# Optimization experiments

Hardware: AMD Instinct MI355X
Metric: run time of the kernel (lower is better)

The kernel has to match this reference:

```python
import jax, jax.numpy as jnp
import numpy as np

B, T, D, H = 4, 2048, 1024, 16
Dh = D // H  # 64


def setup_inputs() -> dict:
    key = jax.random.key(0)
    ks = jax.random.split(key, 12)
    s = 1.0 / np.sqrt(D)
    return {
        "q": jax.random.normal(ks[0], (B, T, D), jnp.float32),
        "k": jax.random.normal(ks[1], (B, T, D), jnp.float32),
        "v": jax.random.normal(ks[2], (B, T, D), jnp.float32),
        "Wq": jax.random.normal(ks[3], (D, D), jnp.float32) * s,
        "bq": jnp.zeros((D,), jnp.float32),
        "Wk": jax.random.normal(ks[4], (D, D), jnp.float32) * s,
        "bk": jnp.zeros((D,), jnp.float32),
        "Wv": jax.random.normal(ks[5], (Dh, D), jnp.float32) * s,
        "bv": jnp.zeros((Dh,), jnp.float32),
        "Wo": jax.random.normal(ks[6], (D, D), jnp.float32) * s,
        "bo": jnp.zeros((D,), jnp.float32),
    }


def reference(q, k, v, Wq, bq, Wk, bk, Wv, bv, Wo, bo):
    # Projections (torch Linear: y = x @ W.T + b)
    Q = (q @ Wq.T + bq).reshape(B, T, H, Dh)   # [B,T,H,Dh]
    K = (k @ Wk.T + bk).reshape(B, T, H, Dh)   # [B,T,H,Dh]
    Vs = v @ Wv.T + bv                         # [B,T,Dh] shared across heads
    scale = 1.0 / np.sqrt(Dh).astype(np.float32)
    scores = jnp.einsum('bqhd,bkhd->bhqk', Q, K) * scale  # [B,H,T,T]
    attn = jax.nn.softmax(scores, axis=-1)
    # shared-V: broadcast V over heads
    out = jnp.einsum('bhqk,bkd->bqhd', attn, Vs)  # [B,T,H,Dh]
    out = out.reshape(B, T, D)
    y = out @ Wo.T + bo                           # [B,T,D]
    return y, attn.mean(axis=1)                   # per-head-averaged attention
```

## Files before the change

### kernel.cpp

```cpp
#include <hip/hip_runtime.h>
#include <cstdint>
#include <cstddef>

typedef __attribute__((ext_vector_type(8))) _Float16 half8;
typedef __attribute__((ext_vector_type(4))) _Float16 half4;
typedef __attribute__((ext_vector_type(4))) float f32x4;

#define DEV static __device__ __forceinline__
#define AS1(p) (const __attribute__((address_space(1))) void*)(p)
#define AS3(p) (__attribute__((address_space(3))) void*)(p)

DEV half8 cvt8(const float* p) {
    f32x4 a = *(const f32x4*)p;
    f32x4 b = *(const f32x4*)(p + 4);
    half8 o;
    o[0] = (_Float16)a[0]; o[1] = (_Float16)a[1];
    o[2] = (_Float16)a[2]; o[3] = (_Float16)a[3];
    o[4] = (_Float16)b[0]; o[5] = (_Float16)b[1];
    o[6] = (_Float16)b[2]; o[7] = (_Float16)b[3];
    return o;
}

__global__ __launch_bounds__(256)
void cvt_kernel(const float* __restrict__ in, _Float16* __restrict__ out, int n8)
{
    int i = blockIdx.x * 256 + threadIdx.x;
    int stride = gridDim.x * 256;
    for (; i < n8; i += stride)
        ((half8*)out)[i] = cvt8(in + (size_t)i * 8);
}

__global__ __launch_bounds__(256)
void opsum_kernel(const _Float16* __restrict__ a, const _Float16* __restrict__ b,
                  _Float16* __restrict__ out, int n8)
{
    int i = blockIdx.x * 256 + threadIdx.x;
    int stride = gridDim.x * 256;
    for (; i < n8; i += stride) {
        half8 x = ((const half8*)a)[i];
        half8 y = ((const half8*)b)[i];
        half8 o;
#pragma unroll
        for (int j = 0; j < 8; j++) o[j] = (_Float16)((float)x[j] + (float)y[j]);
        ((half8*)out)[i] = o;
    }
}

__global__ __launch_bounds__(256)
void combine_kernel(const _Float16* __restrict__ a, const _Float16* __restrict__ b,
                    float* __restrict__ out, int n8)
{
    int i = blockIdx.x * 256 + threadIdx.x;
    int stride = gridDim.x * 256;
    for (; i < n8; i += stride) {
        half8 x = ((const half8*)a)[i];
        half8 y = ((const half8*)b)[i];
        f32x4 o0, o1;
#pragma unroll
        for (int j = 0; j < 4; j++) o0[j] = ((float)x[j] + (float)y[j]) * 0.0625f;
#pragma unroll
        for (int j = 0; j < 4; j++) o1[j] = ((float)x[j + 4] + (float)y[j + 4]) * 0.0625f;
        *(f32x4*)(out + (size_t)i * 8) = o0;
        *(f32x4*)(out + (size_t)i * 8 + 4) = o1;
    }
}

template<bool OUT_F16>
__global__ __launch_bounds__(256, 2)
void gemm16(const _Float16* __restrict__ A, const _Float16* __restrict__ B,
            const float* __restrict__ bias, float scale, void* __restrict__ Cout,
            int M, int N, int K)
{
    __shared__ half8 As[2][512];
    __shared__ half8 Bs[2][512];
    const int tid = threadIdx.x, l = tid & 63, w = tid >> 6;
    const int lr = l & 15, lh = l >> 4;
    const int wm0 = (w >> 1) * 64, wn0 = (w & 1) * 64;
    const int bm0 = blockIdx.x * 128, bn0 = blockIdx.y * 128;
    const int nsteps = K >> 5;

    f32x4 acc[4][4] = {};

#define STAGE(buf, t) do {                                                        \
        int k0 = (t) << 5;                                                        \
        _Pragma("unroll")                                                         \
        for (int q2 = 0; q2 < 2; q2++) {                                          \
            int r = q2 * 64 + l;                                                  \
            __builtin_amdgcn_global_load_lds(                                     \
                AS1(A + (size_t)(bm0 + r) * K + k0 + w * 8),                      \
                AS3(&As[buf][w * 128 + q2 * 64]), 16, 0, 0);                      \
            __builtin_amdgcn_global_load_lds(                                     \
                AS1(B + (size_t)(bn0 + r) * K + k0 + w * 8),                      \
                AS3(&Bs[buf][w * 128 + q2 * 64]), 16, 0, 0);                      \
        }                                                                         \
    } while (0)

    STAGE(0, 0);
    __syncthreads();
    for (int t = 0; t < nsteps; t++) {
        int cur = t & 1;
        if (t + 1 < nsteps) STAGE(cur ^ 1, t + 1);
        half8 a[4], b[4];
#pragma unroll
        for (int m = 0; m < 4; m++) a[m] = As[cur][lh * 128 + wm0 + m * 16 + lr];
#pragma unroll
        for (int n = 0; n < 4; n++) b[n] = Bs[cur][lh * 128 + wn0 + n * 16 + lr];
#pragma unroll
        for (int m = 0; m < 4; m++)
#pragma unroll
            for (int n = 0; n < 4; n++)
                acc[m][n] = __builtin_amdgcn_mfma_f32_16x16x32_f16(a[m], b[n], acc[m][n], 0, 0, 0);
        __syncthreads();
    }
#undef STAGE

#pragma unroll
    for (int m = 0; m < 4; m++)
#pragma unroll
        for (int n = 0; n < 4; n++) {
            int row0 = bm0 + wm0 + m * 16 + lh * 4;
            int col = bn0 + wn0 + n * 16 + lr;
            float bv = bias[col];
#pragma unroll
            for (int j = 0; j < 4; j++) {
                float val = (acc[m][n][j] + bv) * scale;
                int row = row0 + j;
                if constexpr (OUT_F16)
                    ((_Float16*)Cout)[(size_t)row * N + col] = (_Float16)val;
                else
                    ((float*)Cout)[(size_t)row * N + col] = val;
            }
        }
}

template<int BM, int BN, int WR, int WC>
__global__ __launch_bounds__(256, 2)
void gemm_vp(const float* __restrict__ Aptr, const float* __restrict__ Bw,
             const float* __restrict__ bias, _Float16* __restrict__ Cout, int M, int N, int K)
{
    constexpr int BK = 32;
    constexpr int WM = BM / WR, WN = BN / WC;
    constexpr int MF = WM / 16, NF = WN / 16;
    constexpr int LDT = 40;
    __shared__ _Float16 Asl[BM][LDT];
    __shared__ _Float16 Bsl[BN][LDT];

    const int tid = threadIdx.x;
    const int l = tid & 63;
    const int w = tid >> 6;
    const int wr = w / WC, wc = w % WC;
    const int lr = l & 15, lh = l >> 4;
    const int bm0 = blockIdx.y * BM, bn0 = blockIdx.x * BN;

    f32x4 acc[MF][NF] = {};

    for (int k0 = 0; k0 < K; k0 += BK) {
        __syncthreads();
        for (int c = tid; c < BM * 4; c += 256) {
            int row = c >> 2, c8 = (c & 3) << 3;
            *(half8*)&Asl[row][c8] = cvt8(Aptr + (size_t)(bm0 + row) * K + k0 + c8);
        }
        for (int c = tid; c < BN * 4; c += 256) {
            int row = c >> 2, c8 = (c & 3) << 3;
            *(half8*)&Bsl[row][c8] = cvt8(Bw + (size_t)(bn0 + row) * K + k0 + c8);
        }
        __syncthreads();

        half8 a[MF], b[NF];
#pragma unroll
        for (int m = 0; m < MF; m++)
            a[m] = *(const half8*)&Asl[wr * WM + m * 16 + lr][lh * 8];
#pragma unroll
        for (int n = 0; n < NF; n++)
            b[n] = *(const half8*)&Bsl[wc * WN + n * 16 + lr][lh * 8];
#pragma unroll
        for (int m = 0; m < MF; m++)
#pragma unroll
            for (int n = 0; n < NF; n++)
                acc[m][n] = __builtin_amdgcn_mfma_f32_16x16x32_f16(a[m], b[n], acc[m][n], 0, 0, 0);
    }

#pragma unroll
    for (int m = 0; m < MF; m++)
#pragma unroll
        for (int n = 0; n < NF; n++) {
            int row0 = bm0 + wr * WM + m * 16 + lh * 4;
            int col = bn0 + wc * WN + n * 16 + lr;
            float bv = bias[col];
#pragma unroll
            for (int j = 0; j < 4; j++) {
                float val = acc[m][n][j] + bv;
                int row = row0 + j;
                int bi = row >> 11, t = row & 2047;
                Cout[(((size_t)(bi * 64 + col)) << 11) + t] = (_Float16)val;
            }
        }
}

#define LK(dst, kt) do {                                                          \
        const _Float16* kp_ = Kb + (size_t)((kt) * 32) * 1024;                    \
        _Pragma("unroll")                                                         \
        for (int kfr_ = 0; kfr_ < 2; kfr_++)                                      \
            _Pragma("unroll")                                                     \
            for (int dk_ = 0; dk_ < 2; dk_++)                                     \
                dst[kfr_][dk_] = *(const half8*)(kp_ + (size_t)(kfr_ * 16 + lr) * 1024 \
                                                 + ch + dk_ * 32 + lh * 8);       \
    } while (0)

__global__ __launch_bounds__(512, 4)
void stats_kernel(const _Float16* __restrict__ Qh, const _Float16* __restrict__ Kh,
                  float* __restrict__ slp)
{
    const int blk = blockIdx.x;
    const int b = blk & 3;
    const int hg = (blk >> 2) & 1;
    const int q0 = (blk >> 3) << 5;
    const int tid = threadIdx.x;
    const int l = tid & 63, w = tid >> 6;
    const int lr = l & 15, lh = l >> 4;
    const int ch = (hg * 8 + w) * 64;

    const size_t base = (size_t)b * 2048 * 1024;
    const _Float16* Qb = Qh + base;
    const _Float16* Kb = Kh + base;

    half8 qf[2][2];
#pragma unroll
    for (int m = 0; m < 2; m++)
#pragma unroll
        for (int dk = 0; dk < 2; dk++)
            qf[m][dk] = *(const half8*)(Qb + (size_t)(q0 + m * 16 + lr) * 1024
                                        + ch + dk * 32 + lh * 8);

    float sl[2][4] = {};
    half8 ka[2][2], kb2[2][2];

#define SBODY(KF) do {                                                            \
        f32x4 sc[2][2] = {};                                                      \
        _Pragma("unroll")                                                         \
        for (int m = 0; m < 2; m++)                                               \
            _Pragma("unroll")                                                     \
            for (int kfr = 0; kfr < 2; kfr++)                                     \
                _Pragma("unroll")                                                 \
                for (int dk = 0; dk < 2; dk++)                                    \
                    sc[m][kfr] = __builtin_amdgcn_mfma_f32_16x16x32_f16(          \
                        qf[m][dk], KF[kfr][dk], sc[m][kfr], 0, 0, 0);             \
        _Pragma("unroll")                                                         \
        for (int m = 0; m < 2; m++)                                               \
            _Pragma("unroll")                                                     \
            for (int j = 0; j < 4; j++)                                           \
                sl[m][j] += __builtin_amdgcn_exp2f(sc[m][0][j])                   \
                          + __builtin_amdgcn_exp2f(sc[m][1][j]);                  \
    } while (0)

    LK(ka, 0);
    for (int kt = 0; kt < 64; kt += 2) {
        LK(kb2, kt + 1);
        SBODY(ka);
        LK(ka, kt + 2 < 64 ? kt + 2 : 63);
        SBODY(kb2);
    }
#undef SBODY

#pragma unroll
    for (int m = 0; m < 2; m++)
#pragma unroll
        for (int j = 0; j < 4; j++) {
            float s = sl[m][j];
#pragma unroll
            for (int d = 1; d < 16; d <<= 1)
                s += __shfl_xor(s, d, 64);
            if (lr == 0)
                slp[(size_t)(b * 16 + hg * 8 + w) * 2048 + q0 + m * 16 + lh * 4 + j] = s;
        }
}

__global__ __launch_bounds__(512, 4)
void emit_kernel(const _Float16* __restrict__ Qh, const _Float16* __restrict__ Kh,
                 const _Float16* __restrict__ VT, const float* __restrict__ slp,
                 _Float16* __restrict__ attnp, _Float16* __restrict__ Op)
{
    const int blk = blockIdx.x;
    const int b = blk & 3;
    const int ks = (blk >> 2) & 1;
    const int hg = (blk >> 3) & 1;
    const int q0 = (blk >> 4) << 5;
    const int tid = threadIdx.x;
    const int l = tid & 63, w = tid >> 6;
    const int lr = l & 15, lh = l >> 4;
    const int ch = (hg * 8 + w) * 64;

    __shared__ _Float16 Pld[2][8][32][44];

    const size_t base = (size_t)b * 2048 * 1024;
    const _Float16* Qb = Qh + base;
    const _Float16* Kb = Kh + base;

    half8 qf[2][2];
#pragma unroll
    for (int m = 0; m < 2; m++)
#pragma unroll
        for (int dk = 0; dk < 2; dk++)
            qf[m][dk] = *(const half8*)(Qb + (size_t)(q0 + m * 16 + lr) * 1024
                                        + ch + dk * 32 + lh * 8);

    float rinv[2][4];
    {
        const float* sr = slp + (size_t)(b * 16 + hg * 8 + w) * 2048 + q0;
#pragma unroll
        for (int m = 0; m < 2; m++)
#pragma unroll
            for (int j = 0; j < 4; j++)
                rinv[m][j] = 1.0f / sr[m * 16 + lh * 4 + j];
    }

    f32x4 oacc[2][4] = {};
    const int kt0 = ks * 32;
    half8 ka[2][2], kb2[2][2];

#define EBODY(KF, KT, P) do {                                                     \
        const int krow = (KT) * 32;                                               \
        f32x4 sc[2][2] = {};                                                      \
        _Pragma("unroll")                                                         \
        for (int m = 0; m < 2; m++)                                               \
            _Pragma("unroll")                                                     \
            for (int kfr = 0; kfr < 2; kfr++)                                     \
                _Pragma("unroll")                                                 \
                for (int dk = 0; dk < 2; dk++)                                    \
                    sc[m][kfr] = __builtin_amdgcn_mfma_f32_16x16x32_f16(          \
                        qf[m][dk], KF[kfr][dk], sc[m][kfr], 0, 0, 0);             \
        _Pragma("unroll")                                                         \
        for (int m = 0; m < 2; m++)                                               \
            _Pragma("unroll")                                                     \
            for (int kfr = 0; kfr < 2; kfr++)                                     \
                _Pragma("unroll")                                                 \
                for (int j = 0; j < 4; j++) {                                     \
                    float pv = __builtin_amdgcn_exp2f(sc[m][kfr][j]) * rinv[m][j];\
                    Pld[P][w][m * 16 + lh * 4 + j][kfr * 16 + lr] = (_Float16)pv; \
                }                                                                 \
        half8 vf01[2], vf23[2], pa[2];                                            \
        _Pragma("unroll")                                                         \
        for (int dv = 0; dv < 2; dv++)                                            \
            vf01[dv] = *(const half8*)(VT + (((size_t)(b * 64 + dv * 16 + lr)) << 11) + krow + lh * 8); \
        _Pragma("unroll")                                                         \
        for (int m = 0; m < 2; m++) {                                             \
            union { half8 v8; half4 v4[2]; } pu;                                  \
            pu.v4[0] = *(const half4*)&Pld[P][w][m * 16 + lr][lh * 8];            \
            pu.v4[1] = *(const half4*)&Pld[P][w][m * 16 + lr][lh * 8 + 4];        \
            pa[m] = pu.v8;                                                        \
        }                                                                         \
        _Pragma("unroll")                                                         \
        for (int dv = 0; dv < 2; dv++)                                            \
            vf23[dv] = *(const half8*)(VT + (((size_t)(b * 64 + (dv + 2) * 16 + lr)) << 11) + krow + lh * 8); \
        _Pragma("unroll")                                                         \
        for (int m = 0; m < 2; m++)                                               \
            _Pragma("unroll")                                                     \
            for (int dv = 0; dv < 2; dv++)                                        \
                oacc[m][dv] = __builtin_amdgcn_mfma_f32_16x16x32_f16(             \
                    pa[m], vf01[dv], oacc[m][dv], 0, 0, 0);                       \
        _Pragma("unroll")                                                         \
        for (int m = 0; m < 2; m++)                                               \
            _Pragma("unroll")                                                     \
            for (int dv = 0; dv < 2; dv++)                                        \
                oacc[m][dv + 2] = __builtin_amdgcn_mfma_f32_16x16x32_f16(         \
                    pa[m], vf23[dv], oacc[m][dv + 2], 0, 0, 0);                   \
        __syncthreads();                                                          \
        {                                                                         \
            int r = tid >> 4, c2 = (tid & 15) * 2;                                \
            float s0 = 0.f, s1 = 0.f;                                             \
            _Pragma("unroll")                                                     \
            for (int ww = 0; ww < 8; ww++) {                                      \
                s0 += (float)Pld[P][ww][r][c2];                                   \
                s1 += (float)Pld[P][ww][r][c2 + 1];                               \
            }                                                                     \
            union { _Float16 h[2]; uint32_t u; } pk;                              \
            pk.h[0] = (_Float16)s0; pk.h[1] = (_Float16)s1;                       \
            __builtin_nontemporal_store(pk.u, (uint32_t*)(attnp                   \
                + (size_t)hg * 16777216 + (((size_t)(b * 2048 + q0 + r)) << 11)   \
                + krow + c2));                                                    \
        }                                                                         \
    } while (0)

    LK(ka, kt0);
    for (int i = 0; i < 32; i += 2) {
        LK(kb2, kt0 + i + 1);
        EBODY(ka, kt0 + i, 0);
        LK(ka, kt0 + (i + 2 < 32 ? i + 2 : 31));
        EBODY(kb2, kt0 + i + 1, 1);
    }
#undef EBODY

    _Float16* op = Op + (size_t)ks * 8388608 + base;
#pragma unroll
    for (int m = 0; m < 2; m++)
#pragma unroll
        for (int dv = 0; dv < 4; dv++)
#pragma unroll
            for (int j = 0; j < 4; j++) {
                int row = q0 + m * 16 + lh * 4 + j;
                int col = ch + dv * 16 + lr;
                __builtin_nontemporal_store((_Float16)oacc[m][dv][j],
                                            &op[(size_t)row * 1024 + col]);
            }
}

extern "C" void kernel_launch(void* const* d_in, const int* in_sizes, int n_in,
                              void* d_out, int out_size, void* d_ws, size_t ws_size,
                              hipStream_t stream)
{
    const float* q  = (const float*)d_in[0];
    const float* k  = (const float*)d_in[1];
    const float* v  = (const float*)d_in[2];
    const float* Wq = (const float*)d_in[3];
    const float* bq = (const float*)d_in[4];
    const float* Wk = (const float*)d_in[5];
    const float* bk = (const float*)d_in[6];
    const float* Wv = (const float*)d_in[7];
    const float* bv = (const float*)d_in[8];
    const float* Wo = (const float*)d_in[9];
    const float* bo = (const float*)d_in[10];

    float* y = (float*)d_out;
    float* attn_mean = y + (size_t)4 * 2048 * 1024;

    uint8_t* ws = (uint8_t*)d_ws;
    _Float16* Qh  = (_Float16*)(ws);
    _Float16* Kh  = (_Float16*)(ws + 16777216);
    _Float16* VT  = (_Float16*)(ws + 33554432);
    _Float16* Wqc = (_Float16*)(ws + 34603008);
    _Float16* Wkc = (_Float16*)(ws + 36700160);
    _Float16* Woc = (_Float16*)(ws + 38797312);
    _Float16* qc  = (_Float16*)(ws + 40894464);
    _Float16* kc  = (_Float16*)(ws + 57671680);
    _Float16* Op  = qc;
    _Float16* attnp = (_Float16*)(ws + 74448896);
    float*    slp = (float*)(ws + 34603008);

    const float QS = 0.125f * 1.44269504088896340736f;

    cvt_kernel<<<dim3(1024), dim3(256), 0, stream>>>(q, qc, 1048576);
    cvt_kernel<<<dim3(1024), dim3(256), 0, stream>>>(k, kc, 1048576);
    cvt_kernel<<<dim3(512),  dim3(256), 0, stream>>>(Wq, Wqc, 131072);
    cvt_kernel<<<dim3(512),  dim3(256), 0, stream>>>(Wk, Wkc, 131072);
    cvt_kernel<<<dim3(512),  dim3(256), 0, stream>>>(Wo, Woc, 131072);

    gemm16<true><<<dim3(64, 8), dim3(256), 0, stream>>>(qc, Wqc, bq, QS, Qh, 8192, 1024, 1024);
    gemm16<true><<<dim3(64, 8), dim3(256), 0, stream>>>(kc, Wkc, bk, 1.0f, Kh, 8192, 1024, 1024);
    gemm_vp<128, 64, 4, 1><<<dim3(1, 64), dim3(256), 0, stream>>>(v, Wv, bv, VT, 8192, 64, 1024);

    stats_kernel<<<dim3(512), dim3(512), 0, stream>>>(Qh, Kh, slp);
    emit_kernel<<<dim3(1024), dim3(512), 0, stream>>>(Qh, Kh, VT, slp, attnp, Op);

    combine_kernel<<<dim3(2048), dim3(256), 0, stream>>>(
        attnp, attnp + (size_t)16777216, attn_mean, 2097152);
    opsum_kernel<<<dim3(1024), dim3(256), 0, stream>>>(Op, Op + (size_t)8388608, Op, 1048576);

    gemm16<false><<<dim3(64, 8), dim3(256), 0, stream>>>(Op, Woc, bo, 1.0f, y, 8192, 1024, 1024);
}
```

Measured before the change: 626.5 us.

## Drop key-split in emit kernel and merge conversion launches

```diff
diff --git a/kernel.cpp b/kernel.cpp
--- a/kernel.cpp
+++ b/kernel.cpp
@@ -22,27 +22,28 @@
 }
 
 __global__ __launch_bounds__(256)
-void cvt_kernel(const float* __restrict__ in, _Float16* __restrict__ out, int n8)
+void cvt2_kernel(const float* __restrict__ a, _Float16* __restrict__ oa,
+                 const float* __restrict__ b, _Float16* __restrict__ ob, int n8)
 {
     int i = blockIdx.x * 256 + threadIdx.x;
     int stride = gridDim.x * 256;
-    for (; i < n8; i += stride)
-        ((half8*)out)[i] = cvt8(in + (size_t)i * 8);
+    for (; i < 2 * n8; i += stride) {
+        if (i < n8) ((half8*)oa)[i] = cvt8(a + (size_t)i * 8);
+        else        ((half8*)ob)[i - n8] = cvt8(b + (size_t)(i - n8) * 8);
+    }
 }
 
 __global__ __launch_bounds__(256)
-void opsum_kernel(const _Float16* __restrict__ a, const _Float16* __restrict__ b,
-                  _Float16* __restrict__ out, int n8)
+void cvt3_kernel(const float* __restrict__ a, _Float16* __restrict__ oa,
+                 const float* __restrict__ b, _Float16* __restrict__ ob,
+                 const float* __restrict__ c, _Float16* __restrict__ oc, int n8)
 {
     int i = blockIdx.x * 256 + threadIdx.x;
     int stride = gridDim.x * 256;
-    for (; i < n8; i += stride) {
-        half8 x = ((const half8*)a)[i];
-        half8 y = ((const half8*)b)[i];
-        half8 o;
-#pragma unroll
-        for (int j = 0; j < 8; j++) o[j] = (_Float16)((float)x[j] + (float)y[j]);
-        ((half8*)out)[i] = o;
+    for (; i < 3 * n8; i += stride) {
+        if (i < n8)           ((half8*)oa)[i] = cvt8(a + (size_t)i * 8);
+        else if (i < 2 * n8)  ((half8*)ob)[i - n8] = cvt8(b + (size_t)(i - n8) * 8);
+        else                  ((half8*)oc)[i - 2 * n8] = cvt8(c + (size_t)(i - 2 * n8) * 8);
     }
 }
 
@@ -282,9 +283,8 @@
 {
     const int blk = blockIdx.x;
     const int b = blk & 3;
-    const int ks = (blk >> 2) & 1;
-    const int hg = (blk >> 3) & 1;
-    const int q0 = (blk >> 4) << 5;
+    const int hg = (blk >> 2) & 1;
+    const int q0 = (blk >> 3) << 5;
     const int tid = threadIdx.x;
     const int l = tid & 63, w = tid >> 6;
     const int lr = l & 15, lh = l >> 4;
@@ -315,7 +315,6 @@
     }
 
     f32x4 oacc[2][4] = {};
-    const int kt0 = ks * 32;
     half8 ka[2][2], kb2[2][2];
 
 #define EBODY(KF, KT, P) do {                                                     \
@@ -381,16 +380,16 @@
         }                                                                         \
     } while (0)
 
-    LK(ka, kt0);
-    for (int i = 0; i < 32; i += 2) {
-        LK(kb2, kt0 + i + 1);
-        EBODY(ka, kt0 + i, 0);
-        LK(ka, kt0 + (i + 2 < 32 ? i + 2 : 31));
-        EBODY(kb2, kt0 + i + 1, 1);
+    LK(ka, 0);
+    for (int i = 0; i < 64; i += 2) {
+        LK(kb2, i + 1);
+        EBODY(ka, i, 0);
+        LK(ka, i + 2 < 64 ? i + 2 : 63);
+        EBODY(kb2, i + 1, 1);
     }
 #undef EBODY
 
-    _Float16* op = Op + (size_t)ks * 8388608 + base;
+    _Float16* op = Op + base;
 #pragma unroll
     for (int m = 0; m < 2; m++)
 #pragma unroll
@@ -399,8 +398,7 @@
             for (int j = 0; j < 4; j++) {
                 int row = q0 + m * 16 + lh * 4 + j;
                 int col = ch + dv * 16 + lr;
-                __builtin_nontemporal_store((_Float16)oacc[m][dv][j],
-                                            &op[(size_t)row * 1024 + col]);
+                op[(size_t)row * 1024 + col] = (_Float16)oacc[m][dv][j];
             }
 }
 
@@ -438,22 +436,18 @@
 
     const float QS = 0.125f * 1.44269504088896340736f;
 
-    cvt_kernel<<<dim3(1024), dim3(256), 0, stream>>>(q, qc, 1048576);
-    cvt_kernel<<<dim3(1024), dim3(256), 0, stream>>>(k, kc, 1048576);
-    cvt_kernel<<<dim3(512),  dim3(256), 0, stream>>>(Wq, Wqc, 131072);
-    cvt_kernel<<<dim3(512),  dim3(256), 0, stream>>>(Wk, Wkc, 131072);
-    cvt_kernel<<<dim3(512),  dim3(256), 0, stream>>>(Wo, Woc, 131072);
+    cvt2_kernel<<<dim3(2048), dim3(256), 0, stream>>>(q, qc, k, kc, 1048576);
+    cvt3_kernel<<<dim3(512),  dim3(256), 0, stream>>>(Wq, Wqc, Wk, Wkc, Wo, Woc, 131072);
 
     gemm16<true><<<dim3(64, 8), dim3(256), 0, stream>>>(qc, Wqc, bq, QS, Qh, 8192, 1024, 1024);
     gemm16<true><<<dim3(64, 8), dim3(256), 0, stream>>>(kc, Wkc, bk, 1.0f, Kh, 8192, 1024, 1024);
     gemm_vp<128, 64, 4, 1><<<dim3(1, 64), dim3(256), 0, stream>>>(v, Wv, bv, VT, 8192, 64, 1024);
 
     stats_kernel<<<dim3(512), dim3(512), 0, stream>>>(Qh, Kh, slp);
-    emit_kernel<<<dim3(1024), dim3(512), 0, stream>>>(Qh, Kh, VT, slp, attnp, Op);
+    emit_kernel<<<dim3(512), dim3(512), 0, stream>>>(Qh, Kh, VT, slp, attnp, Op);
 
     combine_kernel<<<dim3(2048), dim3(256), 0, stream>>>(
         attnp, attnp + (size_t)16777216, attn_mean, 2097152);
-    opsum_kernel<<<dim3(1024), dim3(256), 0, stream>>>(Op, Op + (size_t)8388608, Op, 1048576);
 
     gemm16<false><<<dim3(64, 8), dim3(256), 0, stream>>>(Op, Woc, bo, 1.0f, y, 8192, 1024, 1024);
 }
```

Measured after the change: 604.3 us. 3.5% less time.
